# Performance work log

Measured on AMD Instinct MI355X. Metric: run time of the kernel, lower is better.

## Reference

```python
import jax, jax.numpy as jnp
import numpy as np

CONF_THRESHOLD = 0.01
LOC_VAR = 0.1   # variance for center offsets
SIZE_VAR = 0.2  # variance for width/height


def decode_boxes(pred_loc, dboxes):
    # pred_loc: (B, N, 4) offsets; dboxes: (N, 4) as (cx, cy, w, h)
    d_cxcy = dboxes[:, :2]  # (N, 2)
    d_wh = dboxes[:, 2:]    # (N, 2)
    cxcy = d_cxcy + pred_loc[:, :, :2] * LOC_VAR * d_wh          # (B, N, 2)
    wh = d_wh * jnp.exp(pred_loc[:, :, 2:] * SIZE_VAR)           # (B, N, 2)
    # centered (cx, cy, w, h) -> corners (xmin, ymin, xmax, ymax)
    return jnp.concatenate([cxcy - wh * 0.5, cxcy + wh * 0.5], axis=-1)


def setup_inputs() -> dict:
    key = jax.random.key(0)
    k1, k2 = jax.random.split(key)
    predicts = jax.random.normal(k1, (64, 24564, 85), dtype=jnp.float32)
    dboxes = jax.random.uniform(k2, (24564, 4), dtype=jnp.float32, minval=0.05, maxval=0.95)
    return {"predicts": predicts, "dboxes": dboxes}


def reference(predicts, dboxes):
    pred_loc = predicts[:, :, :4]   # (B, N, 4)
    pred_conf = predicts[:, :, 4:]  # (B, N, C)
    inf_loc = decode_boxes(pred_loc, dboxes)          # (B, N, 4)
    indicator = pred_conf > CONF_THRESHOLD            # (B, N, C) bool
    return inf_loc, indicator
```

## Files before the change

### kernel.cpp

```cpp
#include <hip/hip_runtime.h>

#define CONF_THRESHOLD 0.01f
#define LOC_VAR 0.1f
#define SIZE_VAR 0.2f

__global__ __launch_bounds__(256) void infbox_fused(
    const float* __restrict__ pred,
    const float4* __restrict__ dboxes,
    float* __restrict__ out,
    int NA, unsigned int R, unsigned int M , unsigned int T) {
    unsigned int t = blockIdx.x * blockDim.x + threadIdx.x;
    if (t >= T) return;

    unsigned int j = t * 4u;
    if (j < M) {
        unsigned int a = j / 81u;
        unsigned int c = j - a * 81u;
        float r[4];
#pragma unroll
        for (int k = 0; k < 4; ++k) {
            unsigned int jj = j + (unsigned int)k;
            float v = (jj < M) ? pred[(size_t)a * 85u + 4u + c] : 0.0f;
            r[k] = (v > CONF_THRESHOLD) ? 1.0f : 0.0f;
            if (++c == 81u) { c = 0u; ++a; }
        }
        float4* out2 = (float4*)(out + (size_t)R * 4u);
        float4 o2;
        o2.x = r[0]; o2.y = r[1]; o2.z = r[2]; o2.w = r[3];
        out2[t] = o2;
    }

    if (t < R) {
        size_t base = (size_t)t * 85u;
        float l0 = pred[base + 0];
        float l1 = pred[base + 1];
        float l2 = pred[base + 2];
        float l3 = pred[base + 3];
        float4 db = dboxes[t % (unsigned int)NA];
        float cx = db.x + l0 * LOC_VAR * db.z;
        float cy = db.y + l1 * LOC_VAR * db.w;
        float w  = db.z * expf(l2 * SIZE_VAR);
        float h  = db.w * expf(l3 * SIZE_VAR);
        float4 o1;
        o1.x = cx - w * 0.5f;
        o1.y = cy - h * 0.5f;
        o1.z = cx + w * 0.5f;
        o1.w = cy + h * 0.5f;
        ((float4*)out)[t] = o1;
    }
}

extern "C" void kernel_launch(void* const* d_in, const int* in_sizes, int n_in,
                              void* d_out, int out_size, void* d_ws, size_t ws_size,
                              hipStream_t stream) {
    const float* predicts = (const float*)d_in[0];
    const float* dboxes   = (const float*)d_in[1];
    float* out = (float*)d_out;

    const int NA = in_sizes[1] / 4;
    const unsigned int R = (unsigned int)(out_size / 85);
    const unsigned int M = R * 81u;
    const unsigned int quads = (M + 3u) / 4u;
    const unsigned int T = (quads > R) ? quads : R;

    const int block = 256;
    unsigned int grid = (T + (unsigned int)block - 1u) / (unsigned int)block;
    infbox_fused<<<grid, block, 0, stream>>>(predicts, (const float4*)dboxes,
                                             out, NA, R, M, T);
}
```

Measured before the change: 933.9 us.

## Stage 48-row input tiles in LDS with float4 loads, then emit boxes and indicators

Each block now copies a contiguous tile of 48 anchor rows (48*85 floats) into shared memory using coalesced float4 loads. Box decode and the conf-threshold indicator are then computed from LDS, and the indicator output is written with scalar coalesced stores. This replaces the scattered, misaligned per-thread gathers from global memory in both phases. The costs are scalar indicator stores instead of float4 stores, a block barrier, and lower occupancy from about 16KB of LDS per block.

```diff
diff --git a/kernel.cpp b/kernel.cpp
--- a/kernel.cpp
+++ b/kernel.cpp
@@ -4,49 +4,95 @@
 #define LOC_VAR 0.1f
 #define SIZE_VAR 0.2f
 
-__global__ __launch_bounds__(256) void infbox_fused(
+#define CH 48
+#define CHF (CH * 85)
+#define CHF4 (CHF / 4)
+#define CCONF (CH * 81)
+
+__global__ __launch_bounds__(256, 8) void infbox_tiled(
+    const float4* __restrict__ pred4,
     const float* __restrict__ pred,
     const float4* __restrict__ dboxes,
     float* __restrict__ out,
-    int NA, unsigned int R, unsigned int M , unsigned int T) {
-    unsigned int t = blockIdx.x * blockDim.x + threadIdx.x;
-    if (t >= T) return;
+    int NA, unsigned int R) {
+    __shared__ float lds[CHF];
 
-    unsigned int j = t * 4u;
-    if (j < M) {
-        unsigned int a = j / 81u;
-        unsigned int c = j - a * 81u;
-        float r[4];
+    const unsigned int tid = threadIdx.x;
+    const unsigned int blk = blockIdx.x;
+    const size_t rowbase = (size_t)blk * CH;
+    const size_t fbase = rowbase * 85u;
+    const size_t F = (size_t)R * 85u;
+
+    if (fbase + CHF <= F) {
+        const size_t b4 = fbase >> 2;
+        float4* lds4 = (float4*)lds;
 #pragma unroll
-        for (int k = 0; k < 4; ++k) {
-            unsigned int jj = j + (unsigned int)k;
-            float v = (jj < M) ? pred[(size_t)a * 85u + 4u + c] : 0.0f;
-            r[k] = (v > CONF_THRESHOLD) ? 1.0f : 0.0f;
-            if (++c == 81u) { c = 0u; ++a; }
+        for (unsigned int i = 0; i < 4; ++i) {
+            unsigned int idx = tid + i * 256u;
+            if (idx < CHF4) lds4[idx] = pred4[b4 + idx];
         }
-        float4* out2 = (float4*)(out + (size_t)R * 4u);
-        float4 o2;
-        o2.x = r[0]; o2.y = r[1]; o2.z = r[2]; o2.w = r[3];
-        out2[t] = o2;
+    } else {
+        for (unsigned int i = tid; i < CHF; i += 256u) {
+            size_t f = fbase + i;
+            lds[i] = (f < F) ? pred[f] : 0.0f;
+        }
+    }
+    __syncthreads();
+
+    if (tid < CH) {
+        size_t row = rowbase + tid;
+        if (row < R) {
+            unsigned int la = tid * 85u;
+            float l0 = lds[la + 0];
+            float l1 = lds[la + 1];
+            float l2 = lds[la + 2];
+            float l3 = lds[la + 3];
+            unsigned int r32 = (unsigned int)row;
+            float4 db = dboxes[r32 % (unsigned int)NA];
+            float cx = db.x + l0 * LOC_VAR * db.z;
+            float cy = db.y + l1 * LOC_VAR * db.w;
+            float w  = db.z * expf(l2 * SIZE_VAR);
+            float h  = db.w * expf(l3 * SIZE_VAR);
+            float4 o;
+            o.x = cx - w * 0.5f;
+            o.y = cy - h * 0.5f;
+            o.z = cx + w * 0.5f;
+            o.w = cy + h * 0.5f;
+            ((float4*)out)[row] = o;
+        }
     }
 
-    if (t < R) {
-        size_t base = (size_t)t * 85u;
-        float l0 = pred[base + 0];
-        float l1 = pred[base + 1];
-        float l2 = pred[base + 2];
-        float l3 = pred[base + 3];
-        float4 db = dboxes[t % (unsigned int)NA];
-        float cx = db.x + l0 * LOC_VAR * db.z;
-        float cy = db.y + l1 * LOC_VAR * db.w;
-        float w  = db.z * expf(l2 * SIZE_VAR);
-        float h  = db.w * expf(l3 * SIZE_VAR);
-        float4 o1;
-        o1.x = cx - w * 0.5f;
-        o1.y = cy - h * 0.5f;
-        o1.z = cx + w * 0.5f;
-        o1.w = cy + h * 0.5f;
-        ((float4*)out)[t] = o1;
+    {
+        const size_t M = (size_t)R * 81u;
+        const size_t gc0 = (size_t)blk * CCONF;
+        float* __restrict__ outc = out + (size_t)R * 4u;
+
+        if (gc0 + CCONF <= M) {
+            unsigned int a = tid / 81u;
+            unsigned int c = tid - a * 81u;
+            unsigned int addr = a * 85u + 4u + c;
+#pragma unroll
+            for (unsigned int i = 0; i < 16; ++i) {
+                unsigned int e = tid + i * 256u;
+                if (i < 15 || e < CCONF) {
+                    float v = lds[addr];
+                    outc[gc0 + e] = (v > CONF_THRESHOLD) ? 1.0f : 0.0f;
+                }
+                c += 13u;
+                addr += 268u;
+                if (c >= 81u) { c -= 81u; addr += 4u; }
+            }
+        } else {
+            for (unsigned int e = tid; e < CCONF; e += 256u) {
+                size_t g = gc0 + e;
+                if (g < M) {
+                    unsigned int aa = e / 81u;
+                    unsigned int cc = e - aa * 81u;
+                    float v = lds[aa * 85u + 4u + cc];
+                    outc[g] = (v > CONF_THRESHOLD) ? 1.0f : 0.0f;
+                }
+            }
+        }
     }
 }
 
@@ -59,12 +105,8 @@
 
     const int NA = in_sizes[1] / 4;
     const unsigned int R = (unsigned int)(out_size / 85);
-    const unsigned int M = R * 81u;
-    const unsigned int quads = (M + 3u) / 4u;
-    const unsigned int T = (quads > R) ? quads : R;
 
-    const int block = 256;
-    unsigned int grid = (T + (unsigned int)block - 1u) / (unsigned int)block;
-    infbox_fused<<<grid, block, 0, stream>>>(predicts, (const float4*)dboxes,
-                                             out, NA, R, M, T);
+    const unsigned int grid = (R + (unsigned int)CH - 1u) / (unsigned int)CH;
+    infbox_tiled<<<grid, 256, 0, stream>>>((const float4*)predicts, predicts,
+                                           (const float4*)dboxes, out, NA, R);
 }
```

Result: faster. 866.6 us (-7.2%).
